# Optimization experiments

Measured on AMD Instinct MI355X. Metric: run time of the kernel, lower is better.

Reference implementation:

```python
import jax, jax.numpy as jnp
import numpy as np

N = 50000
NEG_SLOPE = 0.2


def leaky_relu(x, slope=NEG_SLOPE):
    return jnp.where(x >= 0, x, slope * x)


def gat_conv(x, edge_index, W, a_src, a_dst, bias):
    """PyG GATConv, heads=1, add_self_loops=True.
    x: [N, Fin], edge_index: [2, E] (row 0 = source j, row 1 = target i),
    W: [Fin, Fout], a_src/a_dst: [Fout], bias: [Fout].
    """
    n = x.shape[0]
    # add self loops
    loops = jnp.arange(n, dtype=edge_index.dtype)
    src = jnp.concatenate([edge_index[0], loops])
    dst = jnp.concatenate([edge_index[1], loops])

    xw = x @ W                       # [N, Fout]
    alpha_src = xw @ a_src           # [N]
    alpha_dst = xw @ a_dst           # [N]

    e = leaky_relu(alpha_src[src] + alpha_dst[dst])   # [E+N]
    # segment softmax over edges sharing the same target node
    m = jax.ops.segment_max(e, dst, num_segments=n)   # [N]
    ex = jnp.exp(e - m[dst])
    denom = jax.ops.segment_sum(ex, dst, num_segments=n)  # [N] (>0 via self loops)
    att = ex / denom[dst]                              # [E+N]

    msgs = att[:, None] * xw[src]                      # [E+N, Fout]
    out = jax.ops.segment_sum(msgs, dst, num_segments=n)
    return out + bias


def setup_inputs() -> dict:
    key = jax.random.key(0)
    ks = jax.random.split(key, 12)
    E = 800000
    Fin, H, Fout = 128, 256, 128
    x = jax.random.normal(ks[0], (N, Fin), dtype=jnp.float32)
    edge_index = jax.random.randint(ks[1], (2, E), 0, N, dtype=jnp.int64)
    s = 0.1
    W1 = jax.random.normal(ks[2], (Fin, H), dtype=jnp.float32) * s
    a1_src = jax.random.normal(ks[3], (H,), dtype=jnp.float32) * s
    a1_dst = jax.random.normal(ks[4], (H,), dtype=jnp.float32) * s
    b1 = jax.random.normal(ks[5], (H,), dtype=jnp.float32) * s
    W2 = jax.random.normal(ks[6], (H, Fout), dtype=jnp.float32) * s
    a2_src = jax.random.normal(ks[7], (Fout,), dtype=jnp.float32) * s
    a2_dst = jax.random.normal(ks[8], (Fout,), dtype=jnp.float32) * s
    b2 = jax.random.normal(ks[9], (Fout,), dtype=jnp.float32) * s
    return {"x": x, "edge_index": edge_index, "W1": W1, "a1_src": a1_src,
            "a1_dst": a1_dst, "b1": b1, "W2": W2, "a2_src": a2_src,
            "a2_dst": a2_dst, "b2": b2}


def reference(x, edge_index, W1, a1_src, a1_dst, b1, W2, a2_src, a2_dst, b2):
    h = jax.nn.relu(gat_conv(x, edge_index, W1, a1_src, a1_dst, b1))
    return gat_conv(h, edge_index, W2, a2_src, a2_dst, b2)
```

## Files before the change

kernel.cpp:

```cpp
#include <hip/hip_runtime.h>
#include <hip/hip_bf16.h>

typedef __attribute__((ext_vector_type(8))) short short8;
typedef __attribute__((ext_vector_type(4))) float floatx4;

#define CAP 8192
#define BIN_CH 2048

__device__ __forceinline__ float read_f(const void* p, long long i, int fp32m) {
  return fp32m ? ((const float*)p)[i] : (float)((const __hip_bfloat16*)p)[i];
}
__device__ __forceinline__ float bf2f(unsigned short u) {
  return __uint_as_float((unsigned)u << 16);
}
__device__ __forceinline__ unsigned short f2bf(float f) {
  const unsigned u = __float_as_uint(f);
  return (unsigned short)((u + 0x7fffu + ((u >> 16) & 1u)) >> 16);
}

__device__ __forceinline__ void pack_one(const void* W, unsigned short* Wp, int i,
                                         int K, int NOUT, int m) {
  const int k = i / NOUT, n = i - k * NOUT;
  const int ct = n >> 4, c = n & 15, ks = k >> 5, quad = (k >> 3) & 3, j = k & 7;
  Wp[(((ct * (K / 32) + ks) * 4 + quad) * 16 + c) * 8 + j] = f2bf(read_f(W, i, m));
}

__global__ __launch_bounds__(256) void prep_k(const void* __restrict__ x,
                                              const void* __restrict__ ei,
                                              const void* __restrict__ W1,
                                              const void* __restrict__ a1s,
                                              const void* __restrict__ a1d,
                                              const void* __restrict__ b1,
                                              const void* __restrict__ W2,
                                              const void* __restrict__ a2s,
                                              const void* __restrict__ a2d,
                                              const void* __restrict__ b2,
                                              unsigned short* __restrict__ Wp1,
                                              unsigned short* __restrict__ Wp2,
                                              float* __restrict__ w_as1, float* __restrict__ w_ad1,
                                              float* __restrict__ v_a2s, float* __restrict__ v_a2d,
                                              float* __restrict__ v_b1,  float* __restrict__ v_b2,
                                              int* __restrict__ bkcnt,
                                              int* __restrict__ flags) {
  __shared__ int fl_s[2];
  const int t = threadIdx.x, b = blockIdx.x;
  if (t < 64) {
    const unsigned short w = ((const unsigned short*)x)[t * 2];
    const int ef = (w >> 7) & 0xff;
    const bool bf_ok = (ef >= 90 && ef <= 140);
    const unsigned hi = ((const unsigned*)ei)[t * 2 + 1];
    const unsigned long long bm = __ballot(bf_ok);
    const unsigned long long zm = __ballot(hi == 0u);
    if (t == 0) {
      fl_s[0] = (bm == ~0ull) ? 0 : 1;
      fl_s[1] = (zm == ~0ull) ? 1 : 0;
      if (b == 0) { flags[0] = fl_s[0]; flags[1] = fl_s[1]; }
    }
  }
  __syncthreads();
  const int m = fl_s[0];

  if (b < 128) {
    pack_one(W1, Wp1, b * 256 + t, 128, 256, m);
  } else if (b < 256) {
    pack_one(W2, Wp2, (b - 128) * 256 + t, 256, 128, m);
  } else if (b == 256) {
    if (t < 128) {
      float sa = 0.f, sb = 0.f;
      for (int j = 0; j < 256; ++j) {
        const float w = read_f(W1, (long long)t * 256 + j, m);
        sa = fmaf(w, read_f(a1s, j, m), sa);
        sb = fmaf(w, read_f(a1d, j, m), sb);
      }
      w_as1[t] = sa;
      w_ad1[t] = sb;
    }
  } else if (b == 257) {
    if (t < 128) v_a2s[t] = read_f(a2s, t, m);
    else         v_a2d[t - 128] = read_f(a2d, t - 128, m);
  } else if (b == 258) {
    v_b1[t] = read_f(b1, t, m);
  } else {
    if (t < 128) v_b2[t] = read_f(b2, t, m);
    bkcnt[t] = 0;
  }
}

__device__ __forceinline__ void edge_sd(const void* ei, int e, int E, int i64m, int n,
                                        int& s, int& d) {
  if (e < E) {
    if (i64m) { s = (int)((const long long*)ei)[e]; d = (int)((const long long*)ei)[E + e]; }
    else      { s = ((const int*)ei)[e];            d = ((const int*)ei)[E + e]; }
  } else { s = d = e - E; }
  s = min(max(s, 0), n - 1);
  d = min(max(d, 0), n - 1);
}

__global__ __launch_bounds__(256) void front2_k(const void* __restrict__ x,
                                                const void* __restrict__ ei,
                                                const float* __restrict__ w_as1,
                                                const float* __restrict__ w_ad1,
                                                unsigned short* __restrict__ xb,
                                                float* __restrict__ as_, float* __restrict__ ad_,
                                                unsigned* __restrict__ bpool,
                                                int* __restrict__ bkcnt,
                                                int n, int E, int EN, int nbc) {
  __shared__ int fl_s[2];
  __shared__ unsigned stage[BIN_CH];
  __shared__ unsigned daddr[BIN_CH];
  __shared__ int shA[256], shB[256], shC[256], shD[256];
  __shared__ int vtot_s;
  const int t = threadIdx.x, b = blockIdx.x;

  if (t < 64) {
    const unsigned short w = ((const unsigned short*)x)[t * 2];
    const int ef = (w >> 7) & 0xff;
    const bool bf_ok = (ef >= 90 && ef <= 140);
    const unsigned hi = ((const unsigned*)ei)[t * 2 + 1];
    const unsigned long long bm = __ballot(bf_ok);
    const unsigned long long zm = __ballot(hi == 0u);
    if (t == 0) {
      fl_s[0] = (bm == ~0ull) ? 0 : 1;
      fl_s[1] = (zm == ~0ull) ? 1 : 0;
    }
  }
  __syncthreads();
  const int m = fl_s[0], i64m = fl_s[1];

  if (b < nbc) {
    const int gid = b * 256 + t;
    const int node = gid >> 6, lane = gid & 63;
    if (node >= n) return;
    const long long base = (long long)node * 128 + lane * 2;
    const float v0 = read_f(x, base, m), v1 = read_f(x, base + 1, m);
    ushort2 q;
    q.x = f2bf(v0); q.y = f2bf(v1);
    *(ushort2*)(xb + base) = q;
    float s1 = fmaf(v0, w_as1[lane * 2], v1 * w_as1[lane * 2 + 1]);
    float s2 = fmaf(v0, w_ad1[lane * 2], v1 * w_ad1[lane * 2 + 1]);
    for (int off = 32; off; off >>= 1) {
      s1 += __shfl_down(s1, off);
      s2 += __shfl_down(s2, off);
    }
    if (lane == 0) { as_[node] = s1; ad_[node] = s2; }
  } else {
    const int c0 = (b - nbc) * BIN_CH;
    int* bcnt_s = shA; int* boff_s = shB; int* gbase_s = shC; int* sd = shD;
    bcnt_s[t] = 0;
    __syncthreads();

    unsigned val[BIN_CH / 256];
    int buk[BIN_CH / 256];
#pragma unroll
    for (int i = 0; i < BIN_CH / 256; ++i) {
      const int e = c0 + i * 256 + t;
      if (e < EN) {
        int s, d;
        edge_sd(ei, e, E, i64m, n, s, d);
        buk[i] = d >> 8;
        val[i] = (unsigned)s | ((unsigned)(d & 255) << 16);
        atomicAdd(&bcnt_s[buk[i]], 1);
      } else buk[i] = -1;
    }
    __syncthreads();

    const int c = bcnt_s[t];
    sd[t] = c;
    __syncthreads();
    for (int off = 1; off < 256; off <<= 1) {
      const int v = (t >= off) ? sd[t - off] : 0;
      __syncthreads();
      sd[t] += v;
      __syncthreads();
    }
    boff_s[t] = sd[t] - c;
    if (t == 255) vtot_s = sd[255];
    gbase_s[t] = (c > 0) ? atomicAdd(&bkcnt[t], c) : 0;
    bcnt_s[t] = 0;
    __syncthreads();

#pragma unroll
    for (int i = 0; i < BIN_CH / 256; ++i) {
      if (buk[i] >= 0) {
        const int lp = atomicAdd(&bcnt_s[buk[i]], 1);
        const int si = boff_s[buk[i]] + lp;
        stage[si] = val[i];
        const int gp = gbase_s[buk[i]] + lp;
        daddr[si] = (gp < CAP) ? (unsigned)(buk[i] * CAP + gp) : 0xFFFFFFFFu;
      }
    }
    __syncthreads();

    const int vt = vtot_s;
    for (int idx = t; idx < vt; idx += 256)
      if (daddr[idx] != 0xFFFFFFFFu) bpool[daddr[idx]] = stage[idx];
  }
}

__global__ __launch_bounds__(256) void bucket_csr_k(const unsigned* __restrict__ bpool,
                                                    const int* __restrict__ bkcnt,
                                                    unsigned short* __restrict__ csrc,
                                                    int* __restrict__ start_g,
                                                    int* __restrict__ deg_g, int n) {
  __shared__ int deg_s[256], cur_s[256], sd[256];
  const int t = threadIdx.x, b = blockIdx.x;
  int cnt = bkcnt[b];
  if (cnt > CAP) cnt = CAP;
  deg_s[t] = 0;
  __syncthreads();
  for (int idx = t; idx < cnt; idx += 256) {
    const unsigned v = bpool[b * CAP + idx];
    atomicAdd(&deg_s[(v >> 16) & 255], 1);
  }
  __syncthreads();
  const int dg = deg_s[t];
  sd[t] = dg;
  __syncthreads();
  for (int off = 1; off < 256; off <<= 1) {
    const int v = (t >= off) ? sd[t - off] : 0;
    __syncthreads();
    sd[t] += v;
    __syncthreads();
  }
  const int excl = sd[t] - dg;
  const int node = b * 256 + t;
  if (node < n) { start_g[node] = b * CAP + excl; deg_g[node] = dg; }
  cur_s[t] = excl;
  __syncthreads();
  for (int idx = t; idx < cnt; idx += 256) {
    const unsigned v = bpool[b * CAP + idx];
    const int p = atomicAdd(&cur_s[(v >> 16) & 255], 1);
    csrc[b * CAP + p] = (unsigned short)(v & 0xFFFFu);
  }
}

__device__ __forceinline__ void agg_node(const int start, const int end,
                                         const unsigned short* __restrict__ csrc,
                                         const float* __restrict__ as_, const float adv,
                                         const unsigned short* __restrict__ xw,
                                         const int lane, float* acc) {
  const int slot = lane >> 4, col = lane & 15;
  float dsum = 0.f;
#pragma unroll
  for (int c = 0; c < 8; ++c) acc[c] = 0.f;

  for (int base = start; base < end; base += 64) {
    const int idx = base + lane;
    int s_pre = 0;
    float w_pre = 0.f;
    if (idx < end) {
      s_pre = (int)csrc[idx];
      float v = as_[s_pre] + adv;
      v = (v >= 0.f) ? v : 0.2f * v;
      w_pre = __expf(fminf(v, 60.f));
    }
    dsum += w_pre;
    const int cnt = min(64, end - base);
    int j = 0;
    for (; j + 16 <= cnt; j += 16) {
      int ss0 = __shfl(s_pre, j + slot);
      int ss1 = __shfl(s_pre, j + 4 + slot);
      int ss2 = __shfl(s_pre, j + 8 + slot);
      int ss3 = __shfl(s_pre, j + 12 + slot);
      float ww0 = __shfl(w_pre, j + slot);
      float ww1 = __shfl(w_pre, j + 4 + slot);
      float ww2 = __shfl(w_pre, j + 8 + slot);
      float ww3 = __shfl(w_pre, j + 12 + slot);
      const short8 q0 = *(const short8*)(xw + (size_t)ss0 * 128 + col * 8);
      const short8 q1 = *(const short8*)(xw + (size_t)ss1 * 128 + col * 8);
      const short8 q2 = *(const short8*)(xw + (size_t)ss2 * 128 + col * 8);
      const short8 q3 = *(const short8*)(xw + (size_t)ss3 * 128 + col * 8);
#pragma unroll
      for (int c = 0; c < 8; ++c) {
        acc[c] = fmaf(ww0, bf2f((unsigned short)q0[c]), acc[c]);
        acc[c] = fmaf(ww1, bf2f((unsigned short)q1[c]), acc[c]);
        acc[c] = fmaf(ww2, bf2f((unsigned short)q2[c]), acc[c]);
        acc[c] = fmaf(ww3, bf2f((unsigned short)q3[c]), acc[c]);
      }
    }
    for (; j < cnt; j += 8) {
      const int jj0 = j + slot, jj1 = j + 4 + slot;
      int s0 = __shfl(s_pre, jj0);
      float w0 = __shfl(w_pre, jj0);
      int s1 = __shfl(s_pre, jj1);
      float w1 = __shfl(w_pre, jj1);
      const bool ok0 = (jj0 < cnt), ok1 = (jj1 < cnt);
      s0 = ok0 ? s0 : 0; w0 = ok0 ? w0 : 0.f;
      s1 = ok1 ? s1 : 0; w1 = ok1 ? w1 : 0.f;
      const short8 q0 = *(const short8*)(xw + (size_t)s0 * 128 + col * 8);
      const short8 q1 = *(const short8*)(xw + (size_t)s1 * 128 + col * 8);
#pragma unroll
      for (int c = 0; c < 8; ++c) {
        acc[c] = fmaf(w0, bf2f((unsigned short)q0[c]), acc[c]);
        acc[c] = fmaf(w1, bf2f((unsigned short)q1[c]), acc[c]);
      }
    }
  }
  for (int off = 32; off; off >>= 1) dsum += __shfl_down(dsum, off);
  dsum = __shfl(dsum, 0);
  const float r = 1.f / fmaxf(dsum, 1e-30f);
#pragma unroll
  for (int c = 0; c < 8; ++c) {
    acc[c] += __shfl_xor(acc[c], 16);
    acc[c] += __shfl_xor(acc[c], 32);
    acc[c] *= r;
  }
}

__device__ __forceinline__ int aswz(int row, int colbyte) {
  return (row * 256 + (colbyte ^ ((row & 7) << 4))) >> 1;
}
__device__ __forceinline__ int hswz(int row, int colbyte) {
  return (row * 512 + (colbyte ^ ((row & 7) << 4))) >> 1;
}

__global__ __launch_bounds__(1024) void agg_gemm12_k(const int* __restrict__ start_g,
                                                     const int* __restrict__ deg_g,
                                                     const unsigned short* __restrict__ csrc,
                                                     const float* __restrict__ as_,
                                                     const float* __restrict__ ad_,
                                                     const unsigned short* __restrict__ xb,
                                                     const unsigned short* __restrict__ Wp1,
                                                     const unsigned short* __restrict__ Wp2,
                                                     const float* __restrict__ v_b1,
                                                     const float* __restrict__ v_a2s,
                                                     const float* __restrict__ v_a2d,
                                                     unsigned short* __restrict__ xw2,
                                                     float* __restrict__ as2,
                                                     float* __restrict__ ad2, int n) {
  __shared__ unsigned short lds[16 * 128];
  __shared__ unsigned short hs[16 * 256];
  __shared__ float al_s[16], al_d[16];
  const int wv = threadIdx.x >> 6, lane = threadIdx.x & 63;
  const int slot = lane >> 4, col = lane & 15;
  const int node = blockIdx.x * 16 + wv;

  float acc[8];
  if (node < n) {
    const int start = start_g[node];
    agg_node(start, start + deg_g[node], csrc, as_, ad_[node], xb, lane, acc);
  } else {
#pragma unroll
    for (int c = 0; c < 8; ++c) acc[c] = 0.f;
  }
  if (slot == 0) {
    short8 q;
#pragma unroll
    for (int c = 0; c < 8; ++c) q[c] = (short)f2bf(acc[c]);
    *(short8*)&lds[aswz(wv, col * 16)] = q;
  }
  __syncthreads();

  const int quad = slot, c = col;
  floatx4 g = {0.f, 0.f, 0.f, 0.f};
#pragma unroll
  for (int ks = 0; ks < 4; ++ks) {
    const short8 af = *(const short8*)&lds[aswz(c, ks * 64 + quad * 16)];
    const short8 bf = *(const short8*)(Wp1 + (size_t)((wv * 4 + ks) * 64 + lane) * 8);
    g = __builtin_amdgcn_mfma_f32_16x16x32_bf16(af, bf, g, 0, 0, 0);
  }
  const float bv = v_b1[wv * 16 + c];
#pragma unroll
  for (int r = 0; r < 4; ++r) {
    const float v = g[r] + bv;
    hs[hswz(quad * 4 + r, (wv * 16 + c) * 2)] = f2bf(v > 0.f ? v : 0.f);
  }
  if (threadIdx.x < 16) { al_s[threadIdx.x] = 0.f; al_d[threadIdx.x] = 0.f; }
  __syncthreads();

  const int row0 = blockIdx.x * 16;
  if (wv < 8) {
    floatx4 a2 = {0.f, 0.f, 0.f, 0.f};
#pragma unroll
    for (int ks = 0; ks < 8; ++ks) {
      const short8 af = *(const short8*)&hs[hswz(c, ks * 64 + quad * 16)];
      const short8 bf = *(const short8*)(Wp2 + (size_t)((wv * 8 + ks) * 64 + lane) * 8);
      a2 = __builtin_amdgcn_mfma_f32_16x16x32_bf16(af, bf, a2, 0, 0, 0);
    }
    const float asv = v_a2s[wv * 16 + c], adv = v_a2d[wv * 16 + c];
    float pa_s[4], pa_d[4];
#pragma unroll
    for (int r = 0; r < 4; ++r) {
      pa_s[r] = a2[r] * asv;
      pa_d[r] = a2[r] * adv;
      const int rr = row0 + quad * 4 + r;
      if (rr < n) xw2[(size_t)rr * 128 + wv * 16 + c] = f2bf(a2[r]);
    }
    for (int off = 1; off < 16; off <<= 1) {
#pragma unroll
      for (int r = 0; r < 4; ++r) {
        pa_s[r] += __shfl_xor(pa_s[r], off);
        pa_d[r] += __shfl_xor(pa_d[r], off);
      }
    }
    if (c == 0) {
#pragma unroll
      for (int r = 0; r < 4; ++r) {
        atomicAdd(&al_s[quad * 4 + r], pa_s[r]);
        atomicAdd(&al_d[quad * 4 + r], pa_d[r]);
      }
    }
  }
  __syncthreads();
  if (threadIdx.x < 16) {
    const int rr = row0 + threadIdx.x;
    if (rr < n) { as2[rr] = al_s[threadIdx.x]; ad2[rr] = al_d[threadIdx.x]; }
  }
}

__global__ __launch_bounds__(256) void agg_out_k(const int* __restrict__ start_g,
                                                 const int* __restrict__ deg_g,
                                                 const unsigned short* __restrict__ csrc,
                                                 const float* __restrict__ as_,
                                                 const float* __restrict__ ad_,
                                                 const unsigned short* __restrict__ xw,
                                                 const float* __restrict__ bias,
                                                 void* __restrict__ outp, int n,
                                                 const int* __restrict__ flags) {
  const int gid = blockIdx.x * 256 + threadIdx.x;
  const int node = gid >> 6, lane = gid & 63;
  if (node >= n) return;
  const int slot = lane >> 4, col = lane & 15;
  const int start = start_g[node];
  float acc[8];
  agg_node(start, start + deg_g[node], csrc, as_, ad_[node], xw, lane, acc);
  if (slot == 0) {
    const int c0 = col * 8;
    if (flags[0]) {
      float* o = (float*)outp + (size_t)node * 128 + c0;
      floatx4 q0, q1;
#pragma unroll
      for (int c = 0; c < 4; ++c) {
        q0[c] = acc[c] + bias[c0 + c];
        q1[c] = acc[c + 4] + bias[c0 + 4 + c];
      }
      *(floatx4*)o = q0;
      *(floatx4*)(o + 4) = q1;
    } else {
      short8 q;
#pragma unroll
      for (int c = 0; c < 8; ++c) q[c] = (short)f2bf(acc[c] + bias[c0 + c]);
      *(short8*)((unsigned short*)outp + (size_t)node * 128 + c0) = q;
    }
  }
}

extern "C" void kernel_launch(void* const* d_in, const int* in_sizes, int n_in,
                              void* d_out, int out_size, void* d_ws, size_t ws_size,
                              hipStream_t stream) {
  const void* x   = d_in[0];
  const void* ei  = d_in[1];
  const void* W1  = d_in[2];
  const void* a1s = d_in[3];
  const void* a1d = d_in[4];
  const void* b1  = d_in[5];
  const void* W2  = d_in[6];
  const void* a2s = d_in[7];
  const void* a2d = d_in[8];
  const void* b2  = d_in[9];

  const int N  = in_sizes[0] / 128;
  const int E  = in_sizes[1] / 2;
  const int EN = E + N;
  const int NBUK = (N + 255) / 256;

  unsigned short* B1 = (unsigned short*)d_ws;
  unsigned short* H  = B1 + (size_t)N * 128;
  unsigned short* xw2 = H;
  float* as2 = (float*)(H + (size_t)N * 128);
  float* ad2 = as2 + N;
  float* as_   = (float*)(H + (size_t)N * 256);
  float* ad_   = as_ + N;
  int*   start_g = (int*)(ad_ + N);
  int*   deg_g   = start_g + N;
  int*   bkcnt   = deg_g + N;
  unsigned* bpool = (unsigned*)(bkcnt + 256);
  unsigned short* csrc = (unsigned short*)(bpool + (size_t)NBUK * CAP);
  unsigned short* Wp1 = csrc + (size_t)NBUK * CAP;
  unsigned short* Wp2 = Wp1 + 128 * 256;
  float* vecs  = (float*)(Wp2 + 256 * 128);
  int*   flags = (int*)(vecs + 1152);
  float* w_as1 = vecs,        *w_ad1 = vecs + 128;
  float* v_a2s = vecs + 256,  *v_a2d = vecs + 384;
  float* v_b1  = vecs + 512,  *v_b2  = vecs + 768;

  const int NB = (N * 64 + 255) / 256;
  const int BB = (EN + BIN_CH - 1) / BIN_CH;
  const int AG = (N + 15) / 16;

  prep_k<<<260, 256, 0, stream>>>(x, ei, W1, a1s, a1d, b1, W2, a2s, a2d, b2,
                                  Wp1, Wp2, w_as1, w_ad1, v_a2s, v_a2d, v_b1, v_b2,
                                  bkcnt, flags);

  front2_k<<<NB + BB, 256, 0, stream>>>(x, ei, w_as1, w_ad1, B1, as_, ad_,
                                        bpool, bkcnt, N, E, EN, NB);

  bucket_csr_k<<<NBUK, 256, 0, stream>>>(bpool, bkcnt, csrc, start_g, deg_g, N);

  agg_gemm12_k<<<AG, 1024, 0, stream>>>(start_g, deg_g, csrc, as_, ad_, B1, Wp1, Wp2,
                                        v_b1, v_a2s, v_a2d, xw2, as2, ad2, N);

  agg_out_k<<<NB, 256, 0, stream>>>(start_g, deg_g, csrc, as2, ad2, xw2, v_b2, d_out, N, flags);
}
```

Before: 278.7 us.

## Process 32 nodes per block in fused aggregate+GEMM kernel, reuse weight fragments

The fused layer-1 aggregation plus two-GEMM kernel now handles 32 nodes per 1024-thread block instead of 16. Each wave aggregates two nodes, loads its W1 and W2 MFMA fragments once into registers and reuses them across two row tiles, and all 16 waves now take part in the second GEMM instead of only 8. LDS swizzling is replaced by padded row strides, and the 4-wide unrolled gather loop in agg_node is removed in favour of the 2-wide loop only. This halves weight traffic per node and idle waves, but each wave does serial work for two nodes, and removing the unroll reduces memory-level parallelism in the gather.

```diff
diff --git a/kernel.cpp b/kernel.cpp
--- a/kernel.cpp
+++ b/kernel.cpp
@@ -6,6 +6,7 @@
 
 #define CAP 8192
 #define BIN_CH 2048
+#define NPB 32
 
 __device__ __forceinline__ float read_f(const void* p, long long i, int fp32m) {
   return fp32m ? ((const float*)p)[i] : (float)((const __hip_bfloat16*)p)[i];
@@ -256,29 +257,7 @@
     }
     dsum += w_pre;
     const int cnt = min(64, end - base);
-    int j = 0;
-    for (; j + 16 <= cnt; j += 16) {
-      int ss0 = __shfl(s_pre, j + slot);
-      int ss1 = __shfl(s_pre, j + 4 + slot);
-      int ss2 = __shfl(s_pre, j + 8 + slot);
-      int ss3 = __shfl(s_pre, j + 12 + slot);
-      float ww0 = __shfl(w_pre, j + slot);
-      float ww1 = __shfl(w_pre, j + 4 + slot);
-      float ww2 = __shfl(w_pre, j + 8 + slot);
-      float ww3 = __shfl(w_pre, j + 12 + slot);
-      const short8 q0 = *(const short8*)(xw + (size_t)ss0 * 128 + col * 8);
-      const short8 q1 = *(const short8*)(xw + (size_t)ss1 * 128 + col * 8);
-      const short8 q2 = *(const short8*)(xw + (size_t)ss2 * 128 + col * 8);
-      const short8 q3 = *(const short8*)(xw + (size_t)ss3 * 128 + col * 8);
-#pragma unroll
-      for (int c = 0; c < 8; ++c) {
-        acc[c] = fmaf(ww0, bf2f((unsigned short)q0[c]), acc[c]);
-        acc[c] = fmaf(ww1, bf2f((unsigned short)q1[c]), acc[c]);
-        acc[c] = fmaf(ww2, bf2f((unsigned short)q2[c]), acc[c]);
-        acc[c] = fmaf(ww3, bf2f((unsigned short)q3[c]), acc[c]);
-      }
-    }
-    for (; j < cnt; j += 8) {
+    for (int j = 0; j < cnt; j += 8) {
       const int jj0 = j + slot, jj1 = j + 4 + slot;
       int s0 = __shfl(s_pre, jj0);
       float w0 = __shfl(w_pre, jj0);
@@ -307,13 +286,8 @@
   }
 }
 
-__device__ __forceinline__ int aswz(int row, int colbyte) {
-  return (row * 256 + (colbyte ^ ((row & 7) << 4))) >> 1;
-}
-__device__ __forceinline__ int hswz(int row, int colbyte) {
-  return (row * 512 + (colbyte ^ ((row & 7) << 4))) >> 1;
-}
-
+#define LSTR 136
+#define HSTR 264
 __global__ __launch_bounds__(1024) void agg_gemm12_k(const int* __restrict__ start_g,
                                                      const int* __restrict__ deg_g,
                                                      const unsigned short* __restrict__ csrc,
@@ -328,82 +302,94 @@
                                                      unsigned short* __restrict__ xw2,
                                                      float* __restrict__ as2,
                                                      float* __restrict__ ad2, int n) {
-  __shared__ unsigned short lds[16 * 128];
-  __shared__ unsigned short hs[16 * 256];
-  __shared__ float al_s[16], al_d[16];
+  __shared__ unsigned short lds[NPB * LSTR];
+  __shared__ unsigned short hs[NPB * HSTR];
+  __shared__ float al_s[NPB], al_d[NPB];
   const int wv = threadIdx.x >> 6, lane = threadIdx.x & 63;
   const int slot = lane >> 4, col = lane & 15;
-  const int node = blockIdx.x * 16 + wv;
-
-  float acc[8];
-  if (node < n) {
-    const int start = start_g[node];
-    agg_node(start, start + deg_g[node], csrc, as_, ad_[node], xb, lane, acc);
-  } else {
-#pragma unroll
-    for (int c = 0; c < 8; ++c) acc[c] = 0.f;
-  }
-  if (slot == 0) {
-    short8 q;
-#pragma unroll
-    for (int c = 0; c < 8; ++c) q[c] = (short)f2bf(acc[c]);
-    *(short8*)&lds[aswz(wv, col * 16)] = q;
-  }
+  const int node0 = blockIdx.x * NPB;
+
+#pragma unroll
+  for (int k = 0; k < 2; ++k) {
+    const int rv = wv + 16 * k;
+    const int node = node0 + rv;
+    float acc[8];
+    if (node < n) {
+      const int start = start_g[node];
+      agg_node(start, start + deg_g[node], csrc, as_, ad_[node], xb, lane, acc);
+    } else {
+#pragma unroll
+      for (int c = 0; c < 8; ++c) acc[c] = 0.f;
+    }
+    if (slot == 0) {
+      short8 q;
+#pragma unroll
+      for (int c = 0; c < 8; ++c) q[c] = (short)f2bf(acc[c]);
+      *(short8*)&lds[rv * LSTR + col * 8] = q;
+    }
+  }
+  if (threadIdx.x < NPB) { al_s[threadIdx.x] = 0.f; al_d[threadIdx.x] = 0.f; }
   __syncthreads();
 
   const int quad = slot, c = col;
-  floatx4 g = {0.f, 0.f, 0.f, 0.f};
-#pragma unroll
-  for (int ks = 0; ks < 4; ++ks) {
-    const short8 af = *(const short8*)&lds[aswz(c, ks * 64 + quad * 16)];
-    const short8 bf = *(const short8*)(Wp1 + (size_t)((wv * 4 + ks) * 64 + lane) * 8);
-    g = __builtin_amdgcn_mfma_f32_16x16x32_bf16(af, bf, g, 0, 0, 0);
-  }
+  short8 bf1[4];
+#pragma unroll
+  for (int ks = 0; ks < 4; ++ks)
+    bf1[ks] = *(const short8*)(Wp1 + (size_t)((wv * 4 + ks) * 64 + lane) * 8);
   const float bv = v_b1[wv * 16 + c];
 #pragma unroll
+  for (int rt = 0; rt < 2; ++rt) {
+    floatx4 g = {0.f, 0.f, 0.f, 0.f};
+#pragma unroll
+    for (int ks = 0; ks < 4; ++ks) {
+      const short8 af = *(const short8*)&lds[(rt * 16 + c) * LSTR + ks * 32 + quad * 8];
+      g = __builtin_amdgcn_mfma_f32_16x16x32_bf16(af, bf1[ks], g, 0, 0, 0);
+    }
+#pragma unroll
+    for (int r = 0; r < 4; ++r) {
+      const float v = g[r] + bv;
+      hs[(rt * 16 + quad * 4 + r) * HSTR + wv * 16 + c] = f2bf(v > 0.f ? v : 0.f);
+    }
+  }
+  __syncthreads();
+
+  const int ct = wv & 7, rt2 = wv >> 3;
+  short8 bf2[8];
+#pragma unroll
+  for (int ks = 0; ks < 8; ++ks)
+    bf2[ks] = *(const short8*)(Wp2 + (size_t)((ct * 8 + ks) * 64 + lane) * 8);
+  floatx4 a2 = {0.f, 0.f, 0.f, 0.f};
+#pragma unroll
+  for (int ks = 0; ks < 8; ++ks) {
+    const short8 af = *(const short8*)&hs[(rt2 * 16 + c) * HSTR + ks * 32 + quad * 8];
+    a2 = __builtin_amdgcn_mfma_f32_16x16x32_bf16(af, bf2[ks], a2, 0, 0, 0);
+  }
+  const float asv = v_a2s[ct * 16 + c], adv = v_a2d[ct * 16 + c];
+  float pa_s[4], pa_d[4];
+#pragma unroll
   for (int r = 0; r < 4; ++r) {
-    const float v = g[r] + bv;
-    hs[hswz(quad * 4 + r, (wv * 16 + c) * 2)] = f2bf(v > 0.f ? v : 0.f);
-  }
-  if (threadIdx.x < 16) { al_s[threadIdx.x] = 0.f; al_d[threadIdx.x] = 0.f; }
-  __syncthreads();
-
-  const int row0 = blockIdx.x * 16;
-  if (wv < 8) {
-    floatx4 a2 = {0.f, 0.f, 0.f, 0.f};
-#pragma unroll
-    for (int ks = 0; ks < 8; ++ks) {
-      const short8 af = *(const short8*)&hs[hswz(c, ks * 64 + quad * 16)];
-      const short8 bf = *(const short8*)(Wp2 + (size_t)((wv * 8 + ks) * 64 + lane) * 8);
-      a2 = __builtin_amdgcn_mfma_f32_16x16x32_bf16(af, bf, a2, 0, 0, 0);
-    }
-    const float asv = v_a2s[wv * 16 + c], adv = v_a2d[wv * 16 + c];
-    float pa_s[4], pa_d[4];
+    pa_s[r] = a2[r] * asv;
+    pa_d[r] = a2[r] * adv;
+    const int rr = node0 + rt2 * 16 + quad * 4 + r;
+    if (rr < n) xw2[(size_t)rr * 128 + ct * 16 + c] = f2bf(a2[r]);
+  }
+  for (int off = 1; off < 16; off <<= 1) {
 #pragma unroll
     for (int r = 0; r < 4; ++r) {
-      pa_s[r] = a2[r] * asv;
-      pa_d[r] = a2[r] * adv;
-      const int rr = row0 + quad * 4 + r;
-      if (rr < n) xw2[(size_t)rr * 128 + wv * 16 + c] = f2bf(a2[r]);
-    }
-    for (int off = 1; off < 16; off <<= 1) {
-#pragma unroll
-      for (int r = 0; r < 4; ++r) {
-        pa_s[r] += __shfl_xor(pa_s[r], off);
-        pa_d[r] += __shfl_xor(pa_d[r], off);
-      }
-    }
-    if (c == 0) {
-#pragma unroll
-      for (int r = 0; r < 4; ++r) {
-        atomicAdd(&al_s[quad * 4 + r], pa_s[r]);
-        atomicAdd(&al_d[quad * 4 + r], pa_d[r]);
-      }
-    }
-  }
-  __syncthreads();
-  if (threadIdx.x < 16) {
-    const int rr = row0 + threadIdx.x;
+      pa_s[r] += __shfl_xor(pa_s[r], off);
+      pa_d[r] += __shfl_xor(pa_d[r], off);
+    }
+  }
+  if (c == 0) {
+#pragma unroll
+    for (int r = 0; r < 4; ++r) {
+      atomicAdd(&al_s[rt2 * 16 + quad * 4 + r], pa_s[r]);
+      atomicAdd(&al_d[rt2 * 16 + quad * 4 + r], pa_d[r]);
+    }
+  }
+  __syncthreads();
+  if (threadIdx.x < NPB) {
+    const int rr = node0 + threadIdx.x;
     if (rr < n) { as2[rr] = al_s[threadIdx.x]; ad2[rr] = al_d[threadIdx.x]; }
   }
 }
@@ -486,7 +472,7 @@
 
   const int NB = (N * 64 + 255) / 256;
   const int BB = (EN + BIN_CH - 1) / BIN_CH;
-  const int AG = (N + 15) / 16;
+  const int AG = (N + NPB - 1) / NPB;
 
   prep_k<<<260, 256, 0, stream>>>(x, ei, W1, a1s, a1d, b1, W2, a2s, a2d, b2,
                                   Wp1, Wp2, w_as1, w_ad1, v_a2s, v_a2d, v_b1, v_b2,
```

Result: faster. 254.5 us (-8.7%).
